# Optimization experiments

Hardware: AMD Instinct MI355X
Metric: run time of the kernel (lower is better)

The kernel has to match this reference:

```python
import jax, jax.numpy as jnp
import numpy as np

B, T, C, H = 8, 512, 1024, 16
N = C // H
DW, DA, DG = 64, 64, 128  # LoRA dims for decay / icl-rate / gate at C=1024

def _ln(x, w, b, eps=1e-5):
    mu = x.mean(-1, keepdims=True)
    var = ((x - mu) ** 2).mean(-1, keepdims=True)
    return (x - mu) * jax.lax.rsqrt(var + eps) * w + b

def _gn_heads(x, w, b, eps=64e-5):
    # GroupNorm(H groups) over channel dim of (B,T,C)
    xh = x.reshape(x.shape[0], x.shape[1], H, N)
    mu = xh.mean(-1, keepdims=True)
    var = ((xh - mu) ** 2).mean(-1, keepdims=True)
    xh = (xh - mu) * jax.lax.rsqrt(var + eps)
    return xh.reshape(x.shape) * w + b

def _shift(x):
    # RWKV time_shift: ZeroPad2d((0,0,1,-1))
    return jnp.concatenate([jnp.zeros_like(x[:, :1]), x[:, :-1]], axis=1)

def _wkv7(r, w_log, k, v, a, b):
    # all (B,T,H,N); state S (B,H,N,N): S = S*diag(exp(-exp(w))) + (S@a)b^T + v k^T; out = S@r
    decay = jnp.exp(-jnp.exp(w_log))
    def step(state, inp):
        r_t, d_t, k_t, v_t, a_t, b_t = inp
        sa = jnp.einsum('bhij,bhj->bhi', state, a_t)
        state = (state * d_t[:, :, None, :]
                 + sa[..., None] * b_t[:, :, None, :]
                 + v_t[..., None] * k_t[:, :, None, :])
        return state, jnp.einsum('bhij,bhj->bhi', state, r_t)
    xs = tuple(jnp.moveaxis(t, 1, 0) for t in (r, decay, k, v, a, b))
    s0 = jnp.zeros((r.shape[0], H, N, N), r.dtype)
    _, out = jax.lax.scan(step, s0, xs)
    return jnp.moveaxis(out, 0, 1)

def reference(x, v_first, ln_pre_w, ln_pre_b, ln_attn_w, ln_attn_b, ln_ffn_w, ln_ffn_b,
              x_r, x_w, x_k, x_v, x_a, x_g, w0, w1, w2, a0, a1, a2, g1, g2,
              k_k, k_a, r_k, W_r, W_k, W_v, W_o, gn_w, gn_b,
              ffn_x_k, W_ffn1, W_ffn2):
    Bx, Tx = x.shape[0], x.shape[1]
    x = _ln(x, ln_pre_w, ln_pre_b)            # pre_norm (layer_idx==0)
    # --- time mixing (RWKV7Attention) ---
    xn = _ln(x, ln_attn_w, ln_attn_b)
    dx = _shift(xn) - xn
    xr = xn + dx * x_r; xw = xn + dx * x_w; xk = xn + dx * x_k
    xv = xn + dx * x_v; xa = xn + dx * x_a; xg = xn + dx * x_g
    r = xr @ W_r
    w_log = -jax.nn.softplus(-(w0 + jnp.tanh(xw @ w1) @ w2)) - 0.5
    k = xk @ W_k
    v = xv @ W_v
    v_first = v                               # layer 0 stores v
    a = jax.nn.sigmoid(a0 + (xa @ a1) @ a2)   # in-context learning rate
    g = jax.nn.sigmoid(xg @ g1) @ g2          # gate
    kk = (k * k_k).reshape(Bx, Tx, H, N)
    kk = kk / jnp.maximum(jnp.linalg.norm(kk, axis=-1, keepdims=True), 1e-12)
    k = k * (1.0 + (a - 1.0) * k_a)
    rh = r.reshape(Bx, Tx, H, N)
    kh = k.reshape(Bx, Tx, H, N)
    vh = v.reshape(Bx, Tx, H, N)
    ah = a.reshape(Bx, Tx, H, N)
    o = _wkv7(rh, w_log.reshape(Bx, Tx, H, N), kh, vh, -kk, kk * ah)
    o = _gn_heads(o.reshape(Bx, Tx, C), gn_w, gn_b)
    o = o + ((rh * kh * r_k).sum(-1, keepdims=True) * vh).reshape(Bx, Tx, C)
    x = x + (o * g) @ W_o                     # residual (dropout p=0)
    # --- channel mixing (RWKV7FeedForward) ---
    xf = _ln(x, ln_ffn_w, ln_ffn_b)
    kf = xf + (_shift(xf) - xf) * ffn_x_k
    x = x + jnp.square(jax.nn.relu(kf @ W_ffn1)) @ W_ffn2
    return x, v_first

def setup_inputs() -> dict:
    key = jax.random.key(0)
    ks = iter(jax.random.split(key, 40))
    def nrm(shape, s=0.02):
        return jax.random.normal(next(ks), shape, jnp.float32) * s
    f32 = jnp.float32
    d = {
        'x': jax.random.normal(next(ks), (B, T, C), f32),
        'v_first': jnp.zeros((B, T, C), f32),
        'ln_pre_w': jnp.ones((C,), f32), 'ln_pre_b': jnp.zeros((C,), f32),
        'ln_attn_w': jnp.ones((C,), f32), 'ln_attn_b': jnp.zeros((C,), f32),
        'ln_ffn_w': jnp.ones((C,), f32), 'ln_ffn_b': jnp.zeros((C,), f32),
        'x_r': nrm((C,), 0.1), 'x_w': nrm((C,), 0.1), 'x_k': nrm((C,), 0.1),
        'x_v': nrm((C,), 0.1), 'x_a': nrm((C,), 0.1), 'x_g': nrm((C,), 0.1),
        'w0': nrm((C,), 0.5), 'w1': nrm((C, DW)), 'w2': nrm((DW, C)),
        'a0': nrm((C,), 0.1), 'a1': nrm((C, DA)), 'a2': nrm((DA, C)),
        'g1': nrm((C, DG)), 'g2': nrm((DG, C)),
        'k_k': 0.85 * jnp.ones((C,), f32) + nrm((C,), 0.05),
        'k_a': jnp.ones((C,), f32),
        'r_k': nrm((H, N), 0.1),
        'W_r': nrm((C, C)), 'W_k': nrm((C, C)), 'W_v': nrm((C, C)), 'W_o': nrm((C, C)),
        'gn_w': jnp.ones((C,), f32), 'gn_b': jnp.zeros((C,), f32),
        'ffn_x_k': nrm((C,), 0.1),
        'W_ffn1': nrm((C, 4 * C)), 'W_ffn2': nrm((4 * C, C)),
    }
    return d
```

## Files before the change

### kernel.cpp

```cpp
#include <hip/hip_runtime.h>

#define Bb 8
#define Tt 512
#define Cc 1024
#define Hh 16
#define Nh 64
#define Mm 4096
#define BTC 4194304
#define DEV __device__ __forceinline__

typedef __attribute__((ext_vector_type(8))) short short8;
typedef __attribute__((ext_vector_type(4))) float f32x4;

DEV unsigned short f2bf(float f) {
  unsigned int u = __builtin_bit_cast(unsigned int, f);
  u += 0x7fffu + ((u >> 16) & 1u);
  return (unsigned short)(u >> 16);
}

template <int CTRL>
DEV float dppadd(float x) {
  int xi = __builtin_bit_cast(int, x);
  int yi = __builtin_amdgcn_update_dpp(0, xi, CTRL, 0xF, 0xF, true);
  return x + __builtin_bit_cast(float, yi);
}

struct TDesc { const float* in; unsigned short* out; int K, N, bstart, nbx; };
struct TPack { TDesc d[12]; };

__global__ __launch_bounds__(256) void kt_transpose_multi(TPack p) {
  __shared__ float tile[32][33];
  const int bid = blockIdx.x;
  int i = 0;
  #pragma unroll
  for (int j = 1; j < 12; ++j) if (bid >= p.d[j].bstart) i = j;
  const float* in = p.d[i].in;
  unsigned short* out = p.d[i].out;
  const int K = p.d[i].K, N = p.d[i].N;
  const int local = bid - p.d[i].bstart;
  const int byq = local / p.d[i].nbx;
  const int bx = (local - byq * p.d[i].nbx) * 32;
  const int by = byq * 32;
  int tx = threadIdx.x, ty = threadIdx.y;
  #pragma unroll
  for (int q = ty; q < 32; q += 8) {
    int kk = by + q, nn = bx + tx;
    tile[q][tx] = (kk < K && nn < N) ? in[(size_t)kk * N + nn] : 0.f;
  }
  __syncthreads();
  #pragma unroll
  for (int q = ty; q < 32; q += 8) {
    int nn = bx + q, kk = by + tx;
    if (nn < N && kk < K) out[(size_t)nn * K + kk] = f2bf(tile[tx][q]);
  }
}

DEV void row_stats(float v0, float v1, float v2, float v3, float* red,
                   float& mu, float& rs, float eps) {
  float s = v0 + v1 + v2 + v3;
  float q = v0 * v0 + v1 * v1 + v2 * v2 + v3 * v3;
  #pragma unroll
  for (int o = 32; o; o >>= 1) { s += __shfl_down(s, o); q += __shfl_down(q, o); }
  int w = threadIdx.x >> 6;
  __syncthreads();
  if ((threadIdx.x & 63) == 0) { red[w] = s; red[4 + w] = q; }
  __syncthreads();
  s = red[0] + red[1] + red[2] + red[3];
  q = red[4] + red[5] + red[6] + red[7];
  mu = s * (1.f / 1024.f);
  float var = q * (1.f / 1024.f) - mu * mu;
  rs = rsqrtf(var + eps);
}

__global__ __launch_bounds__(256) void k1_mix(
    const float* __restrict__ x,
    const float* __restrict__ lnpw, const float* __restrict__ lnpb,
    const float* __restrict__ lnaw, const float* __restrict__ lnab,
    const float* __restrict__ cr, const float* __restrict__ cw,
    const float* __restrict__ ck, const float* __restrict__ cv,
    const float* __restrict__ ca, const float* __restrict__ cg,
    float* __restrict__ xln,
    unsigned short* __restrict__ mR, unsigned short* __restrict__ mW,
    unsigned short* __restrict__ mK, unsigned short* __restrict__ mV,
    unsigned short* __restrict__ mA, unsigned short* __restrict__ mG) {
  __shared__ float red[8];
  const int row = blockIdx.x;
  const int t = row & (Tt - 1);
  const int tid = threadIdx.x;
  const int c = tid * 4;
  const size_t base = (size_t)row * Cc + c;
  float a0 = x[base], a1 = x[base + 1], a2 = x[base + 2], a3 = x[base + 3];
  float mu, rs;
  row_stats(a0, a1, a2, a3, red, mu, rs, 1e-5f);
  float pw0 = lnpw[c], pw1 = lnpw[c + 1], pw2 = lnpw[c + 2], pw3 = lnpw[c + 3];
  float pb0 = lnpb[c], pb1 = lnpb[c + 1], pb2 = lnpb[c + 2], pb3 = lnpb[c + 3];
  float l0 = (a0 - mu) * rs * pw0 + pb0, l1 = (a1 - mu) * rs * pw1 + pb1;
  float l2 = (a2 - mu) * rs * pw2 + pb2, l3 = (a3 - mu) * rs * pw3 + pb3;
  float4 st; st.x = l0; st.y = l1; st.z = l2; st.w = l3;
  *(float4*)(xln + base) = st;
  row_stats(l0, l1, l2, l3, red, mu, rs, 1e-5f);
  float aw0 = lnaw[c], aw1 = lnaw[c + 1], aw2 = lnaw[c + 2], aw3 = lnaw[c + 3];
  float ab0 = lnab[c], ab1 = lnab[c + 1], ab2 = lnab[c + 2], ab3 = lnab[c + 3];
  float n0 = (l0 - mu) * rs * aw0 + ab0, n1 = (l1 - mu) * rs * aw1 + ab1;
  float n2 = (l2 - mu) * rs * aw2 + ab2, n3 = (l3 - mu) * rs * aw3 + ab3;
  float p0 = 0.f, p1 = 0.f, p2 = 0.f, p3 = 0.f;
  if (t > 0) {
    const size_t pb_ = base - Cc;
    float q0 = x[pb_], q1 = x[pb_ + 1], q2 = x[pb_ + 2], q3 = x[pb_ + 3];
    row_stats(q0, q1, q2, q3, red, mu, rs, 1e-5f);
    float e0 = (q0 - mu) * rs * pw0 + pb0, e1 = (q1 - mu) * rs * pw1 + pb1;
    float e2 = (q2 - mu) * rs * pw2 + pb2, e3 = (q3 - mu) * rs * pw3 + pb3;
    row_stats(e0, e1, e2, e3, red, mu, rs, 1e-5f);
    p0 = (e0 - mu) * rs * aw0 + ab0; p1 = (e1 - mu) * rs * aw1 + ab1;
    p2 = (e2 - mu) * rs * aw2 + ab2; p3 = (e3 - mu) * rs * aw3 + ab3;
  }
  float d0 = p0 - n0, d1 = p1 - n1, d2 = p2 - n2, d3 = p3 - n3;
  #define EMIT(cf, dst) { \
    float f0 = cf[c], f1 = cf[c + 1], f2 = cf[c + 2], f3 = cf[c + 3]; \
    ushort4 u; u.x = f2bf(n0 + d0 * f0); u.y = f2bf(n1 + d1 * f1); \
    u.z = f2bf(n2 + d2 * f2); u.w = f2bf(n3 + d3 * f3); \
    *(ushort4*)(dst + base) = u; }
  EMIT(cr, mR) EMIT(cw, mW) EMIT(ck, mK) EMIT(cv, mV) EMIT(ca, mA) EMIT(cg, mG)
  #undef EMIT
}

DEV void gll16(const unsigned short* g, unsigned short* l) {
  __builtin_amdgcn_global_load_lds(
      (const __attribute__((address_space(1))) void*)g,
      (__attribute__((address_space(3))) void*)l, 16, 0, 0);
}

template <int MODE>
DEV void gemm_epi(float z, size_t oi, int col,
                  float* outF, unsigned short* outB,
                  const float* bias, const float* res) {
  if constexpr (MODE == 0) outF[oi] = z;
  else if constexpr (MODE == 1) outB[oi] = f2bf(z);
  else if constexpr (MODE == 2) outB[oi] = f2bf(tanhf(z));
  else if constexpr (MODE == 3) outB[oi] = f2bf(1.f / (1.f + expf(-z)));
  else if constexpr (MODE == 4) { float m = fmaxf(z, 0.f); outB[oi] = f2bf(m * m); }
  else if constexpr (MODE == 5) { z += bias[col]; outF[oi] = 1.f / (1.f + expf(-z)); }
  else if constexpr (MODE == 6) {
    z += bias[col];
    float sg = 1.f / (1.f + expf(-z));
    outF[oi] = expf(-0.6065306597126334f * sg);
  } else { outF[oi] = z + res[oi]; }
}

DEV void gemm_epi_rt(int mode, float z, size_t oi, int col,
                     float* outF, unsigned short* outB, const float* bias) {
  if (mode == 0) outF[oi] = z;
  else if (mode == 1) outB[oi] = f2bf(z);
  else if (mode == 2) outB[oi] = f2bf(tanhf(z));
  else if (mode == 3) outB[oi] = f2bf(1.f / (1.f + expf(-z)));
  else if (mode == 5) { z += bias[col]; outF[oi] = 1.f / (1.f + expf(-z)); }
  else { z += bias[col]; float sg = 1.f / (1.f + expf(-z));
         outF[oi] = expf(-0.6065306597126334f * sg); }
}

template <int MODE>
__global__ __launch_bounds__(256) void kg_gemm64(
    const unsigned short* __restrict__ A, const unsigned short* __restrict__ Bt,
    int M, int Nn, int K,
    float* __restrict__ outF, unsigned short* __restrict__ outB,
    const float* __restrict__ bias, const float* __restrict__ res) {
  __shared__ unsigned short lsA[128 * 32];
  __shared__ unsigned short lsB[64 * 32];
  const int tid = threadIdx.x;
  const int lane = tid & 63;
  const int wave = tid >> 6;
  const int wy = wave >> 1, wx = wave & 1;
  const int m0 = blockIdx.y * 128;
  const int n0 = blockIdx.x * 64;
  const int sl4 = lane >> 2;
  const int sc = (lane & 3) << 3;
  f32x4 acc[4][2];
  #pragma unroll
  for (int i = 0; i < 4; ++i)
    #pragma unroll
    for (int j = 0; j < 2; ++j) { f32x4 z = {0.f, 0.f, 0.f, 0.f}; acc[i][j] = z; }
  const int fr = lane & 15;
  const int fk = (lane >> 4) << 3;
  for (int k0 = 0; k0 < K; k0 += 32) {
    #pragma unroll
    for (int j = 0; j < 2; ++j) {
      const int rb = (wave + j * 4) * 16;
      gll16(A + (size_t)(m0 + rb + sl4) * K + k0 + sc, lsA + rb * 32);
    }
    {
      const int rb = wave * 16;
      int br = n0 + rb + sl4;
      br = br < Nn ? br : Nn - 1;
      gll16(Bt + (size_t)br * K + k0 + sc, lsB + rb * 32);
    }
    __syncthreads();
    short8 af[4], bf[2];
    #pragma unroll
    for (int mt = 0; mt < 4; ++mt)
      af[mt] = *(const short8*)(lsA + (wy * 64 + mt * 16 + fr) * 32 + fk);
    #pragma unroll
    for (int nt = 0; nt < 2; ++nt)
      bf[nt] = *(const short8*)(lsB + (wx * 32 + nt * 16 + fr) * 32 + fk);
    #pragma unroll
    for (int mt = 0; mt < 4; ++mt)
      #pragma unroll
      for (int nt = 0; nt < 2; ++nt)
        acc[mt][nt] = __builtin_amdgcn_mfma_f32_16x16x32_bf16(af[mt], bf[nt], acc[mt][nt], 0, 0, 0);
    __syncthreads();
  }
  const int rbase = (lane >> 4) << 2;
  const int cbase = lane & 15;
  #pragma unroll
  for (int mt = 0; mt < 4; ++mt)
    #pragma unroll
    for (int nt = 0; nt < 2; ++nt)
      #pragma unroll
      for (int rr = 0; rr < 4; ++rr) {
        int row = m0 + wy * 64 + mt * 16 + rbase + rr;
        int col = n0 + wx * 32 + nt * 16 + cbase;
        if (col < Nn)
          gemm_epi<MODE>(acc[mt][nt][rr], (size_t)row * Nn + col, col, outF, outB, bias, res);
      }
}

DEV void gemm_body_rt(const unsigned short* A, const unsigned short* Bt,
                      int Nn, int K,
                      float* outF, unsigned short* outB, const float* bias,
                      unsigned short* lsA, unsigned short* lsB,
                      int m0, int n0, int mode) {
  const int tid = threadIdx.x;
  const int lane = tid & 63;
  const int wave = tid >> 6;
  const int wy = wave >> 1, wx = wave & 1;
  const int sl4 = lane >> 2;
  const int sc = (lane & 3) << 3;
  f32x4 acc[4][2];
  #pragma unroll
  for (int i = 0; i < 4; ++i)
    #pragma unroll
    for (int j = 0; j < 2; ++j) { f32x4 z = {0.f, 0.f, 0.f, 0.f}; acc[i][j] = z; }
  const int fr = lane & 15;
  const int fk = (lane >> 4) << 3;
  for (int k0 = 0; k0 < K; k0 += 32) {
    #pragma unroll
    for (int j = 0; j < 2; ++j) {
      const int rb = (wave + j * 4) * 16;
      gll16(A + (size_t)(m0 + rb + sl4) * K + k0 + sc, lsA + rb * 32);
    }
    {
      const int rb = wave * 16;
      int br = n0 + rb + sl4;
      br = br < Nn ? br : Nn - 1;
      gll16(Bt + (size_t)br * K + k0 + sc, lsB + rb * 32);
    }
    __syncthreads();
    short8 af[4], bf[2];
    #pragma unroll
    for (int mt = 0; mt < 4; ++mt)
      af[mt] = *(const short8*)(lsA + (wy * 64 + mt * 16 + fr) * 32 + fk);
    #pragma unroll
    for (int nt = 0; nt < 2; ++nt)
      bf[nt] = *(const short8*)(lsB + (wx * 32 + nt * 16 + fr) * 32 + fk);
    #pragma unroll
    for (int mt = 0; mt < 4; ++mt)
      #pragma unroll
      for (int nt = 0; nt < 2; ++nt)
        acc[mt][nt] = __builtin_amdgcn_mfma_f32_16x16x32_bf16(af[mt], bf[nt], acc[mt][nt], 0, 0, 0);
    __syncthreads();
  }
  const int rbase = (lane >> 4) << 2;
  const int cbase = lane & 15;
  #pragma unroll
  for (int mt = 0; mt < 4; ++mt)
    #pragma unroll
    for (int nt = 0; nt < 2; ++nt)
      #pragma unroll
      for (int rr = 0; rr < 4; ++rr) {
        int row = m0 + wy * 64 + mt * 16 + rbase + rr;
        int col = n0 + wx * 32 + nt * 16 + cbase;
        if (col < Nn)
          gemm_epi_rt(mode, acc[mt][nt][rr], (size_t)row * Nn + col, col, outF, outB, bias);
      }
}

__global__ __launch_bounds__(256) void kg_lora1(
    const unsigned short* __restrict__ mW, const unsigned short* __restrict__ mA,
    const unsigned short* __restrict__ mG,
    const unsigned short* __restrict__ w1T, const unsigned short* __restrict__ a1T,
    const unsigned short* __restrict__ g1T,
    unsigned short* __restrict__ tmpw, unsigned short* __restrict__ tmpa,
    unsigned short* __restrict__ tmpg) {
  __shared__ unsigned short lsA[128 * 32];
  __shared__ unsigned short lsB[64 * 32];
  const int z = blockIdx.z;
  const unsigned short* A  = z == 0 ? mW : z == 1 ? mA : mG;
  const unsigned short* Bt = z == 0 ? w1T : z == 1 ? a1T : g1T;
  unsigned short* outB     = z == 0 ? tmpw : z == 1 ? tmpa : tmpg;
  const int Nn = z < 2 ? 64 : 128;
  const int n0 = z < 2 ? 0 : (z - 2) * 64;
  const int mode = z == 0 ? 2 : z == 1 ? 1 : 3;
  gemm_body_rt(A, Bt, Nn, 1024, nullptr, outB, nullptr, lsA, lsB,
               blockIdx.y * 128, n0, mode);
}

__global__ __launch_bounds__(256) void kg_lora2(
    const unsigned short* __restrict__ tmpw, const unsigned short* __restrict__ tmpa,
    const unsigned short* __restrict__ tmpg,
    const unsigned short* __restrict__ w2T, const unsigned short* __restrict__ a2T,
    const unsigned short* __restrict__ g2T,
    float* __restrict__ decay, float* __restrict__ aicl, float* __restrict__ gout,
    const float* __restrict__ w0v, const float* __restrict__ a0v) {
  __shared__ unsigned short lsA[128 * 32];
  __shared__ unsigned short lsB[64 * 32];
  const int z = blockIdx.z;
  const unsigned short* A  = z == 0 ? tmpw : z == 1 ? tmpa : tmpg;
  const unsigned short* Bt = z == 0 ? w2T : z == 1 ? a2T : g2T;
  float* outF              = z == 0 ? decay : z == 1 ? aicl : gout;
  const float* bias        = z == 0 ? w0v : z == 1 ? a0v : nullptr;
  const int K = z < 2 ? 64 : 128;
  const int mode = z == 0 ? 6 : z == 1 ? 5 : 0;
  gemm_body_rt(A, Bt, 1024, K, outF, nullptr, bias, lsA, lsB,
               blockIdx.y * 128, blockIdx.x * 64, mode);
}

template <int MODE>
DEV void gemm2_body(const unsigned short* A, const unsigned short* Bt,
                    int Nn, int K,
                    float* outF, unsigned short* outB,
                    const float* bias, const float* res,
                    unsigned short* lsA, unsigned short* lsB,
                    int m0, int n0) {
  const int tid = threadIdx.x;
  const int lane = tid & 63;
  const int wave = tid >> 6;
  const int wy = wave >> 1, wx = wave & 1;
  const int sl4 = lane >> 2;
  const int sc = (lane & 3) << 3;
  f32x4 acc[4][4];
  #pragma unroll
  for (int i = 0; i < 4; ++i)
    #pragma unroll
    for (int j = 0; j < 4; ++j) { f32x4 z = {0.f, 0.f, 0.f, 0.f}; acc[i][j] = z; }
  const int fr = lane & 15;
  const int fk = (lane >> 4) << 3;
  for (int k0 = 0; k0 < K; k0 += 32) {
    #pragma unroll
    for (int j = 0; j < 2; ++j) {
      const int rb = (wave + j * 4) * 16;
      gll16(A + (size_t)(m0 + rb + sl4) * K + k0 + sc, lsA + rb * 32);
      int br = n0 + rb + sl4;
      br = br < Nn ? br : Nn - 1;
      gll16(Bt + (size_t)br * K + k0 + sc, lsB + rb * 32);
    }
    __syncthreads();
    short8 af[4], bf[4];
    #pragma unroll
    for (int mt = 0; mt < 4; ++mt)
      af[mt] = *(const short8*)(lsA + (wy * 64 + mt * 16 + fr) * 32 + fk);
    #pragma unroll
    for (int nt = 0; nt < 4; ++nt)
      bf[nt] = *(const short8*)(lsB + (wx * 64 + nt * 16 + fr) * 32 + fk);
    #pragma unroll
    for (int mt = 0; mt < 4; ++mt)
      #pragma unroll
      for (int nt = 0; nt < 4; ++nt)
        acc[mt][nt] = __builtin_amdgcn_mfma_f32_16x16x32_bf16(af[mt], bf[nt], acc[mt][nt], 0, 0, 0);
    __syncthreads();
  }
  const int rbase = (lane >> 4) << 2;
  const int cbase = lane & 15;
  #pragma unroll
  for (int mt = 0; mt < 4; ++mt)
    #pragma unroll
    for (int nt = 0; nt < 4; ++nt)
      #pragma unroll
      for (int rr = 0; rr < 4; ++rr) {
        int row = m0 + wy * 64 + mt * 16 + rbase + rr;
        int col = n0 + wx * 64 + nt * 16 + cbase;
        if (col < Nn)
          gemm_epi<MODE>(acc[mt][nt][rr], (size_t)row * Nn + col, col, outF, outB, bias, res);
      }
}

template <int MODE>
__global__ __launch_bounds__(256) void kg_gemm2(
    const unsigned short* __restrict__ A, const unsigned short* __restrict__ Bt,
    int M, int Nn, int K,
    float* __restrict__ outF, unsigned short* __restrict__ outB,
    const float* __restrict__ bias, const float* __restrict__ res) {
  __shared__ unsigned short lsA[128 * 32];
  __shared__ unsigned short lsB[128 * 32];
  gemm2_body<MODE>(A, Bt, Nn, K, outF, outB, bias, res, lsA, lsB,
                   blockIdx.y * 128, blockIdx.x * 128);
}

__global__ __launch_bounds__(256) void kg_qkv_fused(
    const unsigned short* __restrict__ A0, const unsigned short* __restrict__ A1,
    const unsigned short* __restrict__ A2,
    const unsigned short* __restrict__ B0, const unsigned short* __restrict__ B1,
    const unsigned short* __restrict__ B2,
    float* __restrict__ rbuf, float* __restrict__ kbuf, float* __restrict__ vout,
    const float* __restrict__ aicl,
    const float* __restrict__ kkc, const float* __restrict__ kac,
    float* __restrict__ awb, float* __restrict__ bwb) {
  __shared__ unsigned short lsA[128 * 32];
  __shared__ unsigned short lsB[128 * 32];
  const int z = blockIdx.z;
  const unsigned short* A = z == 0 ? A0 : z == 1 ? A1 : A2;
  const unsigned short* Bt = z == 0 ? B0 : z == 1 ? B1 : B2;
  const int tid = threadIdx.x;
  const int lane = tid & 63;
  const int wave = tid >> 6;
  const int wy = wave >> 1, wx = wave & 1;
  const int m0 = blockIdx.y * 128;
  const int n0 = blockIdx.x * 128;
  const int sl4 = lane >> 2;
  const int sc = (lane & 3) << 3;
  f32x4 acc[4][4];
  #pragma unroll
  for (int i = 0; i < 4; ++i)
    #pragma unroll
    for (int j = 0; j < 4; ++j) { f32x4 zz = {0.f, 0.f, 0.f, 0.f}; acc[i][j] = zz; }
  const int fr = lane & 15;
  const int fk = (lane >> 4) << 3;
  for (int k0 = 0; k0 < 1024; k0 += 32) {
    #pragma unroll
    for (int j = 0; j < 2; ++j) {
      const int rb = (wave + j * 4) * 16;
      gll16(A + (size_t)(m0 + rb + sl4) * 1024 + k0 + sc, lsA + rb * 32);
      gll16(Bt + (size_t)(n0 + rb + sl4) * 1024 + k0 + sc, lsB + rb * 32);
    }
    __syncthreads();
    short8 af[4], bf[4];
    #pragma unroll
    for (int mt = 0; mt < 4; ++mt)
      af[mt] = *(const short8*)(lsA + (wy * 64 + mt * 16 + fr) * 32 + fk);
    #pragma unroll
    for (int nt = 0; nt < 4; ++nt)
      bf[nt] = *(const short8*)(lsB + (wx * 64 + nt * 16 + fr) * 32 + fk);
    #pragma unroll
    for (int mt = 0; mt < 4; ++mt)
      #pragma unroll
      for (int nt = 0; nt < 4; ++nt)
        acc[mt][nt] = __builtin_amdgcn_mfma_f32_16x16x32_bf16(af[mt], bf[nt], acc[mt][nt], 0, 0, 0);
    __syncthreads();
  }
  const int rbase = (lane >> 4) << 2;
  const int cbase = lane & 15;
  if (z != 1) {
    float* outF = z == 0 ? rbuf : vout;
    #pragma unroll
    for (int mt = 0; mt < 4; ++mt)
      #pragma unroll
      for (int nt = 0; nt < 4; ++nt)
        #pragma unroll
        for (int rr = 0; rr < 4; ++rr) {
          int row = m0 + wy * 64 + mt * 16 + rbase + rr;
          int col = n0 + wx * 64 + nt * 16 + cbase;
          outF[(size_t)row * Cc + col] = acc[mt][nt][rr];
        }
  } else {
    float kkc4[4], kac4[4];
    #pragma unroll
    for (int nt = 0; nt < 4; ++nt) {
      int col = n0 + wx * 64 + nt * 16 + cbase;
      kkc4[nt] = kkc[col];
      kac4[nt] = kac[col];
    }
    #pragma unroll
    for (int mt = 0; mt < 4; ++mt)
      #pragma unroll
      for (int rr = 0; rr < 4; ++rr) {
        int row = m0 + wy * 64 + mt * 16 + rbase + rr;
        float h0 = acc[mt][0][rr] * kkc4[0];
        float h1 = acc[mt][1][rr] * kkc4[1];
        float h2 = acc[mt][2][rr] * kkc4[2];
        float h3 = acc[mt][3][rr] * kkc4[3];
        float ss = (h0 * h0 + h1 * h1) + (h2 * h2 + h3 * h3);
        ss = dppadd<0xB1>(ss);
        ss = dppadd<0x4E>(ss);
        ss = dppadd<0x124>(ss);
        ss = dppadd<0x128>(ss);
        float inv = 1.f / fmaxf(sqrtf(ss), 1e-12f);
        #pragma unroll
        for (int nt = 0; nt < 4; ++nt) {
          int col = n0 + wx * 64 + nt * 16 + cbase;
          size_t oi = (size_t)row * Cc + col;
          float kv = acc[mt][nt][rr];
          float hn = kv * kkc4[nt] * inv;
          float av = aicl[oi];
          awb[oi] = -hn;
          bwb[oi] = hn * av;
          kbuf[oi] = kv * (1.f + (av - 1.f) * kac4[nt]);
        }
      }
  }
}

#define CS 8
__global__ __launch_bounds__(512, 2) void k5_wkv7(
    const float* __restrict__ r, const float* __restrict__ dec,
    const float* __restrict__ k, const float* __restrict__ v,
    const float* __restrict__ aw, const float* __restrict__ bw,
    float* __restrict__ o) {
  const int blk = blockIdx.x;
  const int bh = blk & 127, half = blk >> 7;
  const int b = bh >> 4, h = bh & 15;
  const int tid = threadIdx.x;
  const int lane = tid & 63;
  const int w = tid >> 6;
  const int cg = lane & 15;
  const int rw = lane >> 4;
  const int row = half * 32 + w * 4 + rw;
  const int cb = cg << 2;

  __shared__ float buf[2][6 * CS * 64];

  float S[4];
  #pragma unroll
  for (int j = 0; j < 4; ++j) S[j] = 0.f;

  const size_t base = (size_t)b * Tt * Cc + (size_t)h * Nh;

  const float* sptr = w == 0 ? aw : w == 1 ? dec : w == 2 ? bw
                    : w == 3 ? k  : w == 4 ? r   : v;
  const int srow = lane >> 4;
  const int scol = (lane & 15) << 2;

  uint4 R0, R1;
  #define LOADC(cstart) if (w < 6) { \
    const size_t g0 = base + (size_t)((cstart) + srow) * Cc + scol; \
    R0 = *(const uint4*)(sptr + g0); \
    R1 = *(const uint4*)(sptr + g0 + 4 * Cc); }

  LOADC(0)

  #pragma unroll 1
  for (int c = 0; c < Tt / CS; ++c) {
    float* bp = buf[c & 1];
    if (w < 6) {
      *(uint4*)(bp + w * 512 + (lane << 2)) = R0;
      *(uint4*)(bp + w * 512 + 256 + (lane << 2)) = R1;
    }
    const int cn = (c + 1 < Tt / CS) ? (c + 1) : c;
    LOADC(cn * CS)
    __syncthreads();

    float4 Aq[2], Dq[2], Bq[2], Kq[2], Rq[2];
    float Vv[2];
    #define LOADOPS(slot, ss) { \
      const float* sp_ = bp + (ss) * 64; \
      Aq[slot] = *(const float4*)(sp_ + cb); \
      Dq[slot] = *(const float4*)(sp_ + 512 + cb); \
      Bq[slot] = *(const float4*)(sp_ + 1024 + cb); \
      Kq[slot] = *(const float4*)(sp_ + 1536 + cb); \
      Rq[slot] = *(const float4*)(sp_ + 2048 + cb); \
      Vv[slot] = sp_[2560 + row]; }

    LOADOPS(0, 0)
    #pragma unroll
    for (int s = 0; s < CS; ++s) {
      const int cu = s & 1, nx = cu ^ 1;
      if (s + 1 < CS) LOADOPS(nx, s + 1)

      float4 a4 = Aq[cu];
      float sa = fmaf(S[1], a4.y, S[0] * a4.x) + fmaf(S[3], a4.w, S[2] * a4.z);
      sa = dppadd<0xB1>(sa);
      sa = dppadd<0x4E>(sa);
      sa = dppadd<0x124>(sa);
      sa = dppadd<0x128>(sa);

      const float vv = Vv[cu];
      float4 d4 = Dq[cu], b4 = Bq[cu], k4 = Kq[cu], r4 = Rq[cu];
      S[0] = fmaf(S[0], d4.x, fmaf(vv, k4.x, sa * b4.x));
      float oo = S[0] * r4.x;
      S[1] = fmaf(S[1], d4.y, fmaf(vv, k4.y, sa * b4.y));
      oo = fmaf(S[1], r4.y, oo);
      S[2] = fmaf(S[2], d4.z, fmaf(vv, k4.z, sa * b4.z));
      oo = fmaf(S[2], r4.z, oo);
      S[3] = fmaf(S[3], d4.w, fmaf(vv, k4.w, sa * b4.w));
      oo = fmaf(S[3], r4.w, oo);

      oo = dppadd<0xB1>(oo);
      oo = dppadd<0x4E>(oo);
      oo = dppadd<0x124>(oo);
      oo = dppadd<0x128>(oo);
      if (cg == 0) o[base + (size_t)(c * CS + s) * Cc + row] = oo;
    }
    #undef LOADOPS
  }
  #undef LOADC
}

__global__ __launch_bounds__(256) void k6_out(
    const float* __restrict__ o, const float* __restrict__ r, const float* __restrict__ k,
    const float* __restrict__ v, const float* __restrict__ rk,
    const float* __restrict__ gnw, const float* __restrict__ gnb,
    const float* __restrict__ g, unsigned short* __restrict__ og) {
  const int row = blockIdx.x, tid = threadIdx.x;
  const int c = tid * 4;
  const size_t base = (size_t)row * Cc + c;
  float o0 = o[base], o1 = o[base + 1], o2 = o[base + 2], o3 = o[base + 3];
  float r0 = r[base], r1 = r[base + 1], r2 = r[base + 2], r3 = r[base + 3];
  float k0 = k[base], k1 = k[base + 1], k2 = k[base + 2], k3 = k[base + 3];
  float s = o0 + o1 + o2 + o3;
  float q = o0 * o0 + o1 * o1 + o2 * o2 + o3 * o3;
  float bs = r0 * k0 * rk[c] + r1 * k1 * rk[c + 1] + r2 * k2 * rk[c + 2] + r3 * k3 * rk[c + 3];
  #pragma unroll
  for (int m = 8; m; m >>= 1) {
    s += __shfl_xor(s, m); q += __shfl_xor(q, m); bs += __shfl_xor(bs, m);
  }
  float mu = s * (1.f / 64.f);
  float var = q * (1.f / 64.f) - mu * mu;
  float rs = rsqrtf(var + 64e-5f);
  float v0 = v[base], v1 = v[base + 1], v2 = v[base + 2], v3 = v[base + 3];
  float z0 = (o0 - mu) * rs * gnw[c] + gnb[c] + bs * v0;
  float z1 = (o1 - mu) * rs * gnw[c + 1] + gnb[c + 1] + bs * v1;
  float z2 = (o2 - mu) * rs * gnw[c + 2] + gnb[c + 2] + bs * v2;
  float z3 = (o3 - mu) * rs * gnw[c + 3] + gnb[c + 3] + bs * v3;
  ushort4 u;
  u.x = f2bf(z0 * g[base]); u.y = f2bf(z1 * g[base + 1]);
  u.z = f2bf(z2 * g[base + 2]); u.w = f2bf(z3 * g[base + 3]);
  *(ushort4*)(og + base) = u;
}

__global__ __launch_bounds__(256) void k8_ffnmix(
    const float* __restrict__ x2, const float* __restrict__ lnw, const float* __restrict__ lnb,
    const float* __restrict__ fxk, unsigned short* __restrict__ kf) {
  __shared__ float red[8];
  const int row = blockIdx.x;
  const int t = row & (Tt - 1);
  const int tid = threadIdx.x;
  const int c = tid * 4;
  const size_t base = (size_t)row * Cc + c;
  float a0 = x2[base], a1 = x2[base + 1], a2 = x2[base + 2], a3 = x2[base + 3];
  float mu, rs;
  row_stats(a0, a1, a2, a3, red, mu, rs, 1e-5f);
  float w0 = lnw[c], w1 = lnw[c + 1], w2 = lnw[c + 2], w3 = lnw[c + 3];
  float b0 = lnb[c], b1 = lnb[c + 1], b2 = lnb[c + 2], b3 = lnb[c + 3];
  float f0 = (a0 - mu) * rs * w0 + b0, f1 = (a1 - mu) * rs * w1 + b1;
  float f2 = (a2 - mu) * rs * w2 + b2, f3 = (a3 - mu) * rs * w3 + b3;
  float p0 = 0.f, p1 = 0.f, p2 = 0.f, p3 = 0.f;
  if (t > 0) {
    const size_t pb_ = base - Cc;
    float q0 = x2[pb_], q1 = x2[pb_ + 1], q2 = x2[pb_ + 2], q3 = x2[pb_ + 3];
    row_stats(q0, q1, q2, q3, red, mu, rs, 1e-5f);
    p0 = (q0 - mu) * rs * w0 + b0; p1 = (q1 - mu) * rs * w1 + b1;
    p2 = (q2 - mu) * rs * w2 + b2; p3 = (q3 - mu) * rs * w3 + b3;
  }
  ushort4 u;
  u.x = f2bf(f0 + (p0 - f0) * fxk[c]);
  u.y = f2bf(f1 + (p1 - f1) * fxk[c + 1]);
  u.z = f2bf(f2 + (p2 - f2) * fxk[c + 2]);
  u.w = f2bf(f3 + (p3 - f3) * fxk[c + 3]);
  *(ushort4*)(kf + base) = u;
}

extern "C" void kernel_launch(void* const* d_in, const int* in_sizes, int n_in,
                              void* d_out, int out_size, void* d_ws, size_t ws_size,
                              hipStream_t stream) {
  (void)in_sizes; (void)n_in; (void)out_size; (void)ws_size;
  const float* x    = (const float*)d_in[0];
  const float* lnpw = (const float*)d_in[2];
  const float* lnpb = (const float*)d_in[3];
  const float* lnaw = (const float*)d_in[4];
  const float* lnab = (const float*)d_in[5];
  const float* lnfw = (const float*)d_in[6];
  const float* lnfb = (const float*)d_in[7];
  const float* cxr  = (const float*)d_in[8];
  const float* cxw  = (const float*)d_in[9];
  const float* cxk  = (const float*)d_in[10];
  const float* cxv  = (const float*)d_in[11];
  const float* cxa  = (const float*)d_in[12];
  const float* cxg  = (const float*)d_in[13];
  const float* w0v  = (const float*)d_in[14];
  const float* w1m  = (const float*)d_in[15];
  const float* w2m  = (const float*)d_in[16];
  const float* a0v  = (const float*)d_in[17];
  const float* a1m  = (const float*)d_in[18];
  const float* a2m  = (const float*)d_in[19];
  const float* g1m  = (const float*)d_in[20];
  const float* g2m  = (const float*)d_in[21];
  const float* kkv  = (const float*)d_in[22];
  const float* kav  = (const float*)d_in[23];
  const float* rkv  = (const float*)d_in[24];
  const float* Wr   = (const float*)d_in[25];
  const float* Wk   = (const float*)d_in[26];
  const float* Wv   = (const float*)d_in[27];
  const float* Wo   = (const float*)d_in[28];
  const float* gnw  = (const float*)d_in[29];
  const float* gnb  = (const float*)d_in[30];
  const float* fxk  = (const float*)d_in[31];
  const float* Wf1  = (const float*)d_in[32];
  const float* Wf2  = (const float*)d_in[33];

  char* ws = (char*)d_ws;
  float* outx = (float*)d_out;
  float* vout = outx + BTC;

  size_t off = 0;
  unsigned short* WrT  = (unsigned short*)(ws + off); off += 2097152;
  unsigned short* WkT  = (unsigned short*)(ws + off); off += 2097152;
  unsigned short* WvT  = (unsigned short*)(ws + off); off += 2097152;
  unsigned short* WoT  = (unsigned short*)(ws + off); off += 2097152;
  unsigned short* Wf1T = (unsigned short*)(ws + off); off += 8388608;
  unsigned short* Wf2T = (unsigned short*)(ws + off); off += 8388608;
  unsigned short* w1T  = (unsigned short*)(ws + off); off += 131072;
  unsigned short* w2T  = (unsigned short*)(ws + off); off += 131072;
  unsigned short* a1T  = (unsigned short*)(ws + off); off += 131072;
  unsigned short* a2T  = (unsigned short*)(ws + off); off += 131072;
  unsigned short* g1T  = (unsigned short*)(ws + off); off += 262144;
  unsigned short* g2T  = (unsigned short*)(ws + off); off += 262144;
  float* xln = (float*)(ws + off); off += 16777216;
  unsigned short* mixR = (unsigned short*)(ws + off);
  unsigned short* mixW = (unsigned short*)(ws + off + 8388608);
  unsigned short* mixK = (unsigned short*)(ws + off + 16777216);
  unsigned short* mixV = (unsigned short*)(ws + off + 25165824);
  unsigned short* mixA = (unsigned short*)(ws + off + 33554432);
  unsigned short* mixG = (unsigned short*)(ws + off + 41943040);
  unsigned short* hbuf = (unsigned short*)(ws + off);
  off += 50331648;
  unsigned short* tmpw = (unsigned short*)(ws + off); off += 524288;
  unsigned short* tmpa = (unsigned short*)(ws + off); off += 524288;
  unsigned short* tmpg = (unsigned short*)(ws + off); off += 1048576;
  float* decay = (float*)(ws + off);
  unsigned short* og = (unsigned short*)(ws + off);
  off += 16777216;
  float* aicl = (float*)(ws + off);
  float* obuf = (float*)(ws + off);
  off += 16777216;
  float* gout = (float*)(ws + off); off += 16777216;
  float* rbuf = (float*)(ws + off);
  float* x2   = (float*)(ws + off);
  off += 16777216;
  float* kbuf = (float*)(ws + off); off += 16777216;
  float* awb  = (float*)(ws + off);
  unsigned short* kf = (unsigned short*)(ws + off);
  off += 16777216;
  float* bwb  = (float*)(ws + off); off += 16777216;

  dim3 tb(32, 8);
  TPack tp;
  tp.d[0]  = TDesc{Wr,  WrT,  1024, 1024, 0,     32};
  tp.d[1]  = TDesc{Wk,  WkT,  1024, 1024, 1024,  32};
  tp.d[2]  = TDesc{Wv,  WvT,  1024, 1024, 2048,  32};
  tp.d[3]  = TDesc{Wo,  WoT,  1024, 1024, 3072,  32};
  tp.d[4]  = TDesc{Wf1, Wf1T, 1024, 4096, 4096,  128};
  tp.d[5]  = TDesc{Wf2, Wf2T, 4096, 1024, 8192,  32};
  tp.d[6]  = TDesc{w1m, w1T,  1024, 64,   12288, 2};
  tp.d[7]  = TDesc{w2m, w2T,  64,   1024, 12352, 32};
  tp.d[8]  = TDesc{a1m, a1T,  1024, 64,   12416, 2};
  tp.d[9]  = TDesc{a2m, a2T,  64,   1024, 12480, 32};
  tp.d[10] = TDesc{g1m, g1T,  1024, 128,  12544, 4};
  tp.d[11] = TDesc{g2m, g2T,  128,  1024, 12672, 32};
  kt_transpose_multi<<<12800, tb, 0, stream>>>(tp);

  k1_mix<<<Mm, 256, 0, stream>>>(x, lnpw, lnpb, lnaw, lnab, cxr, cxw, cxk, cxv, cxa, cxg,
                                 xln, mixR, mixW, mixK, mixV, mixA, mixG);

  kg_lora1<<<dim3(1, 32, 4), 256, 0, stream>>>(mixW, mixA, mixG, w1T, a1T, g1T,
                                               tmpw, tmpa, tmpg);
  kg_lora2<<<dim3(16, 32, 3), 256, 0, stream>>>(tmpw, tmpa, tmpg, w2T, a2T, g2T,
                                                decay, aicl, gout, w0v, a0v);

  kg_qkv_fused<<<dim3(8, 32, 3), 256, 0, stream>>>(mixR, mixK, mixV, WrT, WkT, WvT,
                                                   rbuf, kbuf, vout,
                                                   aicl, kkv, kav, awb, bwb);

  k5_wkv7<<<256, 512, 0, stream>>>(rbuf, decay, kbuf, vout, awb, bwb, obuf);
  k6_out<<<Mm, 256, 0, stream>>>(obuf, rbuf, kbuf, vout, rkv, gnw, gnb, gout, og);
  kg_gemm64<7><<<dim3(16, 32), 256, 0, stream>>>(og, WoT, Mm, 1024, 1024, x2, nullptr, nullptr, xln);
  k8_ffnmix<<<Mm, 256, 0, stream>>>(x2, lnfw, lnfb, fxk, kf);
  kg_gemm2<4><<<dim3(32, 32), 256, 0, stream>>>(kf, Wf1T, Mm, 4096, 1024, nullptr, hbuf, nullptr, nullptr);
  kg_gemm64<7><<<dim3(16, 32), 256, 0, stream>>>(hbuf, Wf2T, Mm, 1024, 4096, outx, nullptr, nullptr, x2);
}
```

Measured before the change: 585.8 us.

## Split-K the FFN down-projection into two halves plus residual add kernel

Replaces the FFN2 GEMM (M=4096, N=1024, K=4096) with a split-K variant using 128x128 tiles over two K halves, which writes two fp32 partial results into reused scratch buffers (obuf, gout). A separate elementwise kernel then sums the partials and adds the residual. The goal is more blocks and shorter K loops for better CU occupancy. The cost is an extra fp32 partial write and read plus one more kernel launch.

```diff
diff --git a/kernel.cpp b/kernel.cpp
--- a/kernel.cpp
+++ b/kernel.cpp
@@ -394,6 +394,78 @@
                    blockIdx.y * 128, blockIdx.x * 128);
 }
 
+__global__ __launch_bounds__(256) void kg_ffn2_sk(
+    const unsigned short* __restrict__ A, const unsigned short* __restrict__ Bt,
+    float* __restrict__ p0, float* __restrict__ p1) {
+  __shared__ unsigned short lsA[128 * 32];
+  __shared__ unsigned short lsB[128 * 32];
+  const int Kstride = 4096, Klen = 2048;
+  const int kbase = blockIdx.z * Klen;
+  float* outF = blockIdx.z == 0 ? p0 : p1;
+  const int tid = threadIdx.x;
+  const int lane = tid & 63;
+  const int wave = tid >> 6;
+  const int wy = wave >> 1, wx = wave & 1;
+  const int m0 = blockIdx.y * 128;
+  const int n0 = blockIdx.x * 128;
+  const int sl4 = lane >> 2;
+  const int sc = (lane & 3) << 3;
+  f32x4 acc[4][4];
+  #pragma unroll
+  for (int i = 0; i < 4; ++i)
+    #pragma unroll
+    for (int j = 0; j < 4; ++j) { f32x4 z = {0.f, 0.f, 0.f, 0.f}; acc[i][j] = z; }
+  const int fr = lane & 15;
+  const int fk = (lane >> 4) << 3;
+  for (int k0 = kbase; k0 < kbase + Klen; k0 += 32) {
+    #pragma unroll
+    for (int j = 0; j < 2; ++j) {
+      const int rb = (wave + j * 4) * 16;
+      gll16(A + (size_t)(m0 + rb + sl4) * Kstride + k0 + sc, lsA + rb * 32);
+      gll16(Bt + (size_t)(n0 + rb + sl4) * Kstride + k0 + sc, lsB + rb * 32);
+    }
+    __syncthreads();
+    short8 af[4], bf[4];
+    #pragma unroll
+    for (int mt = 0; mt < 4; ++mt)
+      af[mt] = *(const short8*)(lsA + (wy * 64 + mt * 16 + fr) * 32 + fk);
+    #pragma unroll
+    for (int nt = 0; nt < 4; ++nt)
+      bf[nt] = *(const short8*)(lsB + (wx * 64 + nt * 16 + fr) * 32 + fk);
+    #pragma unroll
+    for (int mt = 0; mt < 4; ++mt)
+      #pragma unroll
+      for (int nt = 0; nt < 4; ++nt)
+        acc[mt][nt] = __builtin_amdgcn_mfma_f32_16x16x32_bf16(af[mt], bf[nt], acc[mt][nt], 0, 0, 0);
+    __syncthreads();
+  }
+  const int rbase = (lane >> 4) << 2;
+  const int cbase = lane & 15;
+  #pragma unroll
+  for (int mt = 0; mt < 4; ++mt)
+    #pragma unroll
+    for (int nt = 0; nt < 4; ++nt)
+      #pragma unroll
+      for (int rr = 0; rr < 4; ++rr) {
+        int row = m0 + wy * 64 + mt * 16 + rbase + rr;
+        int col = n0 + wx * 64 + nt * 16 + cbase;
+        outF[(size_t)row * Cc + col] = acc[mt][nt][rr];
+      }
+}
+
+__global__ __launch_bounds__(256) void k9_add(
+    const float* __restrict__ p0, const float* __restrict__ p1,
+    const float* __restrict__ x2, float* __restrict__ outx) {
+  const size_t i = ((size_t)blockIdx.x * 256 + threadIdx.x) * 4;
+  float4 a = *(const float4*)(p0 + i);
+  float4 b = *(const float4*)(p1 + i);
+  float4 c = *(const float4*)(x2 + i);
+  float4 o;
+  o.x = a.x + b.x + c.x; o.y = a.y + b.y + c.y;
+  o.z = a.z + b.z + c.z; o.w = a.w + b.w + c.w;
+  *(float4*)(outx + i) = o;
+}
+
 __global__ __launch_bounds__(256) void kg_qkv_fused(
     const unsigned short* __restrict__ A0, const unsigned short* __restrict__ A1,
     const unsigned short* __restrict__ A2,
@@ -772,5 +844,6 @@
   kg_gemm64<7><<<dim3(16, 32), 256, 0, stream>>>(og, WoT, Mm, 1024, 1024, x2, nullptr, nullptr, xln);
   k8_ffnmix<<<Mm, 256, 0, stream>>>(x2, lnfw, lnfb, fxk, kf);
   kg_gemm2<4><<<dim3(32, 32), 256, 0, stream>>>(kf, Wf1T, Mm, 4096, 1024, nullptr, hbuf, nullptr, nullptr);
-  kg_gemm64<7><<<dim3(16, 32), 256, 0, stream>>>(hbuf, Wf2T, Mm, 1024, 4096, outx, nullptr, nullptr, x2);
-}
+  kg_ffn2_sk<<<dim3(8, 32, 2), 256, 0, stream>>>(hbuf, Wf2T, obuf, gout);
+  k9_add<<<Mm, 256, 0, stream>>>(obuf, gout, x2, outx);
+}
```

Result: no change. 580.6 us (-0.9%).

## Add triple-buffered swizzled 8-wave GEMM for FFN with split-K atomic residual

Applied to the files above, without the earlier changes.

Replaces the FFN GEMMs with a new 512-thread kernel that uses 128x256 tiles with K=64 steps. It triple-buffers global-to-LDS loads with explicit vmcnt waits, uses XOR-swizzled LDS layout to avoid bank conflicts, and raises wave priority around the MFMA blocks. The second FFN GEMM is split-K by two and accumulates into outx with atomicAdd. outx is pre-seeded with the residual x2 by having the Wo GEMM epilogue write its output to both x2 and outx. This targets latency exposure and low tile reuse in the FFN matmuls, at the cost of float atomics and non-deterministic summation order.

```diff
diff --git a/kernel.cpp b/kernel.cpp
--- a/kernel.cpp
+++ b/kernel.cpp
@@ -133,7 +133,7 @@
 template <int MODE>
 DEV void gemm_epi(float z, size_t oi, int col,
                   float* outF, unsigned short* outB,
-                  const float* bias, const float* res) {
+                  const float* bias, const float* res, float* outF2) {
   if constexpr (MODE == 0) outF[oi] = z;
   else if constexpr (MODE == 1) outB[oi] = f2bf(z);
   else if constexpr (MODE == 2) outB[oi] = f2bf(tanhf(z));
@@ -144,7 +144,8 @@
     z += bias[col];
     float sg = 1.f / (1.f + expf(-z));
     outF[oi] = expf(-0.6065306597126334f * sg);
-  } else { outF[oi] = z + res[oi]; }
+  } else if constexpr (MODE == 7) { outF[oi] = z + res[oi]; }
+  else { float v = z + res[oi]; outF[oi] = v; outF2[oi] = v; }
 }
 
 DEV void gemm_epi_rt(int mode, float z, size_t oi, int col,
@@ -163,7 +164,8 @@
     const unsigned short* __restrict__ A, const unsigned short* __restrict__ Bt,
     int M, int Nn, int K,
     float* __restrict__ outF, unsigned short* __restrict__ outB,
-    const float* __restrict__ bias, const float* __restrict__ res) {
+    const float* __restrict__ bias, const float* __restrict__ res,
+    float* __restrict__ outF2) {
   __shared__ unsigned short lsA[128 * 32];
   __shared__ unsigned short lsB[64 * 32];
   const int tid = threadIdx.x;
@@ -219,7 +221,7 @@
         int row = m0 + wy * 64 + mt * 16 + rbase + rr;
         int col = n0 + wx * 32 + nt * 16 + cbase;
         if (col < Nn)
-          gemm_epi<MODE>(acc[mt][nt][rr], (size_t)row * Nn + col, col, outF, outB, bias, res);
+          gemm_epi<MODE>(acc[mt][nt][rr], (size_t)row * Nn + col, col, outF, outB, bias, res, outF2);
       }
 }
 
@@ -324,49 +326,92 @@
 }
 
 template <int MODE>
-DEV void gemm2_body(const unsigned short* A, const unsigned short* Bt,
-                    int Nn, int K,
-                    float* outF, unsigned short* outB,
-                    const float* bias, const float* res,
-                    unsigned short* lsA, unsigned short* lsB,
-                    int m0, int n0) {
+__global__ __launch_bounds__(512, 1) void kg_gemm8p(
+    const unsigned short* __restrict__ A, const unsigned short* __restrict__ Bt,
+    int Nn, int Kstride, int Klen,
+    float* __restrict__ outF, unsigned short* __restrict__ outB) {
+  __shared__ unsigned short lds[3 * 24576];
   const int tid = threadIdx.x;
   const int lane = tid & 63;
   const int wave = tid >> 6;
-  const int wy = wave >> 1, wx = wave & 1;
-  const int sl4 = lane >> 2;
-  const int sc = (lane & 3) << 3;
+  const int wm = wave >> 2, wn = wave & 3;
+  const int m0 = blockIdx.y * 128;
+  const int n0 = blockIdx.x * 256;
+  const int kbase = blockIdx.z * Klen;
+  const int ntile = Klen / 64;
+  const int fr = lane & 15;
+  const int fkb = (lane >> 4) << 4;
+
+  int arow[2], acolb[2], brow[4], bcolb[4];
+  #pragma unroll
+  for (int i = 0; i < 2; ++i) {
+    int off = i * 8192 + tid * 16;
+    int r = off >> 7;
+    arow[i] = r; acolb[i] = (off & 127) ^ ((r & 7) << 4);
+  }
+  #pragma unroll
+  for (int i = 0; i < 4; ++i) {
+    int off = i * 8192 + tid * 16;
+    int r = off >> 7;
+    brow[i] = r; bcolb[i] = (off & 127) ^ ((r & 7) << 4);
+  }
+
+  #define STAGE(t_) { \
+    int tc = (t_) < ntile ? (t_) : ntile - 1; \
+    unsigned short* lb_ = lds + ((t_) % 3) * 24576; \
+    const int kk = kbase + tc * 64; \
+    _Pragma("unroll") \
+    for (int i = 0; i < 2; ++i) \
+      gll16(A + (size_t)(m0 + arow[i]) * Kstride + kk + (acolb[i] >> 1), \
+            lb_ + i * 4096 + wave * 512); \
+    _Pragma("unroll") \
+    for (int i = 0; i < 4; ++i) \
+      gll16(Bt + (size_t)(n0 + brow[i]) * Kstride + kk + (bcolb[i] >> 1), \
+            lb_ + 8192 + i * 4096 + wave * 512); \
+  }
+
   f32x4 acc[4][4];
   #pragma unroll
   for (int i = 0; i < 4; ++i)
     #pragma unroll
     for (int j = 0; j < 4; ++j) { f32x4 z = {0.f, 0.f, 0.f, 0.f}; acc[i][j] = z; }
-  const int fr = lane & 15;
-  const int fk = (lane >> 4) << 3;
-  for (int k0 = 0; k0 < K; k0 += 32) {
-    #pragma unroll
-    for (int j = 0; j < 2; ++j) {
-      const int rb = (wave + j * 4) * 16;
-      gll16(A + (size_t)(m0 + rb + sl4) * K + k0 + sc, lsA + rb * 32);
-      int br = n0 + rb + sl4;
-      br = br < Nn ? br : Nn - 1;
-      gll16(Bt + (size_t)br * K + k0 + sc, lsB + rb * 32);
+
+  STAGE(0)
+  STAGE(1)
+  asm volatile("s_waitcnt vmcnt(6)" ::: "memory");
+  __syncthreads();
+
+  for (int t = 0; t < ntile; ++t) {
+    STAGE(t + 2)
+    const unsigned short* lb = lds + (t % 3) * 24576;
+    #pragma unroll
+    for (int ks = 0; ks < 2; ++ks) {
+      short8 af[4], bf[4];
+      #pragma unroll
+      for (int mt = 0; mt < 4; ++mt) {
+        int r = wm * 64 + mt * 16 + fr;
+        int byt = (ks * 64 + fkb) ^ ((r & 7) << 4);
+        af[mt] = *(const short8*)(lb + r * 64 + (byt >> 1));
+      }
+      #pragma unroll
+      for (int nt = 0; nt < 4; ++nt) {
+        int r = wn * 64 + nt * 16 + fr;
+        int byt = (ks * 64 + fkb) ^ ((r & 7) << 4);
+        bf[nt] = *(const short8*)(lb + 8192 + r * 64 + (byt >> 1));
+      }
+      __builtin_amdgcn_s_setprio(1);
+      #pragma unroll
+      for (int mt = 0; mt < 4; ++mt)
+        #pragma unroll
+        for (int nt = 0; nt < 4; ++nt)
+          acc[mt][nt] = __builtin_amdgcn_mfma_f32_16x16x32_bf16(af[mt], bf[nt], acc[mt][nt], 0, 0, 0);
+      __builtin_amdgcn_s_setprio(0);
     }
+    asm volatile("s_waitcnt vmcnt(6)" ::: "memory");
     __syncthreads();
-    short8 af[4], bf[4];
-    #pragma unroll
-    for (int mt = 0; mt < 4; ++mt)
-      af[mt] = *(const short8*)(lsA + (wy * 64 + mt * 16 + fr) * 32 + fk);
-    #pragma unroll
-    for (int nt = 0; nt < 4; ++nt)
-      bf[nt] = *(const short8*)(lsB + (wx * 64 + nt * 16 + fr) * 32 + fk);
-    #pragma unroll
-    for (int mt = 0; mt < 4; ++mt)
-      #pragma unroll
-      for (int nt = 0; nt < 4; ++nt)
-        acc[mt][nt] = __builtin_amdgcn_mfma_f32_16x16x32_bf16(af[mt], bf[nt], acc[mt][nt], 0, 0, 0);
-    __syncthreads();
-  }
+  }
+  #undef STAGE
+
   const int rbase = (lane >> 4) << 2;
   const int cbase = lane & 15;
   #pragma unroll
@@ -375,23 +420,13 @@
     for (int nt = 0; nt < 4; ++nt)
       #pragma unroll
       for (int rr = 0; rr < 4; ++rr) {
-        int row = m0 + wy * 64 + mt * 16 + rbase + rr;
-        int col = n0 + wx * 64 + nt * 16 + cbase;
-        if (col < Nn)
-          gemm_epi<MODE>(acc[mt][nt][rr], (size_t)row * Nn + col, col, outF, outB, bias, res);
+        int row = m0 + wm * 64 + mt * 16 + rbase + rr;
+        int col = n0 + wn * 64 + nt * 16 + cbase;
+        size_t oi = (size_t)row * Nn + col;
+        float z = acc[mt][nt][rr];
+        if constexpr (MODE == 4) { float m = fmaxf(z, 0.f); outB[oi] = f2bf(m * m); }
+        else atomicAdd(outF + oi, z);
       }
-}
-
-template <int MODE>
-__global__ __launch_bounds__(256) void kg_gemm2(
-    const unsigned short* __restrict__ A, const unsigned short* __restrict__ Bt,
-    int M, int Nn, int K,
-    float* __restrict__ outF, unsigned short* __restrict__ outB,
-    const float* __restrict__ bias, const float* __restrict__ res) {
-  __shared__ unsigned short lsA[128 * 32];
-  __shared__ unsigned short lsB[128 * 32];
-  gemm2_body<MODE>(A, Bt, Nn, K, outF, outB, bias, res, lsA, lsB,
-                   blockIdx.y * 128, blockIdx.x * 128);
 }
 
 __global__ __launch_bounds__(256) void kg_qkv_fused(
@@ -769,8 +804,8 @@
 
   k5_wkv7<<<256, 512, 0, stream>>>(rbuf, decay, kbuf, vout, awb, bwb, obuf);
   k6_out<<<Mm, 256, 0, stream>>>(obuf, rbuf, kbuf, vout, rkv, gnw, gnb, gout, og);
-  kg_gemm64<7><<<dim3(16, 32), 256, 0, stream>>>(og, WoT, Mm, 1024, 1024, x2, nullptr, nullptr, xln);
+  kg_gemm64<9><<<dim3(16, 32), 256, 0, stream>>>(og, WoT, Mm, 1024, 1024, x2, nullptr, nullptr, xln, outx);
   k8_ffnmix<<<Mm, 256, 0, stream>>>(x2, lnfw, lnfb, fxk, kf);
-  kg_gemm2<4><<<dim3(32, 32), 256, 0, stream>>>(kf, Wf1T, Mm, 4096, 1024, nullptr, hbuf, nullptr, nullptr);
-  kg_gemm64<7><<<dim3(16, 32), 256, 0, stream>>>(hbuf, Wf2T, Mm, 1024, 4096, outx, nullptr, nullptr, x2);
-}
+  kg_gemm8p<4><<<dim3(16, 32, 1), 512, 0, stream>>>(kf, Wf1T, 4096, 1024, 1024, nullptr, hbuf);
+  kg_gemm8p<8><<<dim3(4, 32, 2), 512, 0, stream>>>(hbuf, Wf2T, 1024, 4096, 2048, outx, nullptr);
+}
```

New measurement: 572.6 us. 1.02x faster.
